# Kernel optimization log

Measured on AMD Instinct MI355X. Metric: run time of the kernel, lower is better.

Reference implementation:

```python
import jax, jax.numpy as jnp
import numpy as np

D_MODEL = 1024
N_HEADS = 16
N_KV_HEADS = 4
HEAD_DIM = 64   # d_model // total_n_heads
KEY_DIM = 64    # defaults to head_dim
N_REP = N_HEADS // N_KV_HEADS
ATTN_SCALE = 1.0 / np.sqrt(HEAD_DIM)
B, S = 2, 2048


def apply_rope(x, cos, sin):
    # x: [B,S,H,Dh]; cos/sin: [S,Dh//2]; pairs are (x[2j], x[2j+1]) per llama-style apply_rotary_emb
    xr, xi = x[..., ::2], x[..., 1::2]
    c = cos[None, :, None, :]
    s = sin[None, :, None, :]
    out_r = xr * c - xi * s
    out_i = xr * s + xi * c
    return jnp.stack([out_r, out_i], axis=-1).reshape(x.shape)


def setup_inputs() -> dict:
    key = jax.random.key(0)
    ks = jax.random.split(key, 7)
    query = jax.random.normal(ks[0], (B, S, D_MODEL), jnp.float32)
    k_in = jax.random.normal(ks[1], (B, S, D_MODEL), jnp.float32)
    v_in = jax.random.normal(ks[2], (B, S, D_MODEL), jnp.float32)
    # real RoPE frequency tables (theta=10000)
    inv_freq = 1.0 / (10000.0 ** (np.arange(0, KEY_DIM, 2, dtype=np.float32) / KEY_DIM))
    ang = np.outer(np.arange(S, dtype=np.float32), inv_freq)  # [S, KEY_DIM//2]
    freqs_cos = jnp.asarray(np.cos(ang), jnp.float32)
    freqs_sin = jnp.asarray(np.sin(ang), jnp.float32)
    sc = D_MODEL ** -0.5
    wq = jax.random.normal(ks[3], (N_HEADS * KEY_DIM, D_MODEL), jnp.float32) * sc
    wk = jax.random.normal(ks[4], (N_KV_HEADS * KEY_DIM, D_MODEL), jnp.float32) * sc
    wv = jax.random.normal(ks[5], (N_KV_HEADS * HEAD_DIM, D_MODEL), jnp.float32) * sc
    wo = jax.random.normal(ks[6], (N_HEADS * HEAD_DIM, N_HEADS * HEAD_DIM), jnp.float32) * sc
    return {"query": query, "key": k_in, "value": v_in,
            "freqs_cos": freqs_cos, "freqs_sin": freqs_sin,
            "wq": wq, "wk": wk, "wv": wv, "wo": wo}


def reference(query, key, value, freqs_cos, freqs_sin, wq, wk, wv, wo):
    b, sq, _ = query.shape
    sk = key.shape[1]
    xq = (query @ wq.T).reshape(b, sq, N_HEADS, KEY_DIM)
    xk = (key @ wk.T).reshape(b, sk, N_KV_HEADS, KEY_DIM)
    xv = (value @ wv.T).reshape(b, sk, N_KV_HEADS, HEAD_DIM)
    xq = apply_rope(xq, freqs_cos, freqs_sin)
    xk = apply_rope(xk, freqs_cos, freqs_sin)
    # GQA: repeat kv heads (equivalent to torch repeat_kv expand+reshape)
    xk = jnp.repeat(xk, N_REP, axis=2)
    xv = jnp.repeat(xv, N_REP, axis=2)
    scores = jnp.einsum('bqhd,bkhd->bhqk', xq, xk) * ATTN_SCALE
    causal = jnp.tril(jnp.ones((sq, sk), dtype=bool))
    scores = jnp.where(causal[None, None, :, :], scores, -jnp.inf)
    attn = jax.nn.softmax(scores, axis=-1)
    out = jnp.einsum('bhqk,bkhd->bqhd', attn, xv).reshape(b, sq, N_HEADS * HEAD_DIM)
    return out @ wo.T
```

## Files before the change

kernel.cpp:

```cpp
#include <hip/hip_runtime.h>

#define DM 1024
#define NHEADS 16
#define NKVH 4
#define HDIM 64
#define NB 2
#define SEQ 2048
#define MTOK (NB*SEQ)

typedef __attribute__((ext_vector_type(4))) float f32x4;
typedef __attribute__((ext_vector_type(8))) short short8;
typedef unsigned short u16;
typedef unsigned int u32;

__device__ __forceinline__ u16 f2b(float f) {
  u32 i; __builtin_memcpy(&i, &f, 4);
  u32 r = i + 0x7fffu + ((i >> 16) & 1u);
  return (u16)(r >> 16);
}
__device__ __forceinline__ u32 cvtpk(float a, float b) {
  u32 r; asm("v_cvt_pk_bf16_f32 %0, %1, %2" : "=v"(r) : "v"(a), "v"(b)); return r;
}
__device__ __forceinline__ float fexp2(float x) {
  float r; asm("v_exp_f32 %0, %1" : "=v"(r) : "v"(x)); return r;
}
__device__ __forceinline__ void gload16(const void* g, void* l) {
  __builtin_amdgcn_global_load_lds((const __attribute__((address_space(1))) u32*)g,
                                   (__attribute__((address_space(3))) u32*)l, 16, 0, 0);
}

__device__ __forceinline__ void cvt8(const float* __restrict__ src, u16* __restrict__ dst, int i) {
  float4 a = *(const float4*)(src + i);
  float4 b = *(const float4*)(src + i + 4);
  uint4 pk;
  pk.x = cvtpk(a.x, a.y);
  pk.y = cvtpk(a.z, a.w);
  pk.z = cvtpk(b.x, b.y);
  pk.w = cvtpk(b.z, b.w);
  *(uint4*)(dst + i) = pk;
}

__global__ __launch_bounds__(256) void cvt_all(const float* __restrict__ q, const float* __restrict__ k,
                                               const float* __restrict__ v, const float* __restrict__ wq,
                                               const float* __restrict__ wk, const float* __restrict__ wv,
                                               const float* __restrict__ wo, u16* oq, u16* ok, u16* ov,
                                               u16* owq, u16* owk, u16* owv, u16* owo) {
  const int ACT = (MTOK * DM) / 2048;
  const int BIG = (DM * DM) / 2048;
  const int SML = (256 * DM) / 2048;
  int bid = blockIdx.x;
  const float* s; u16* d;
  if (bid < ACT) { s = q; d = oq; }
  else if (bid < 2 * ACT) { s = k; d = ok; bid -= ACT; }
  else if (bid < 3 * ACT) { s = v; d = ov; bid -= 2 * ACT; }
  else {
    bid -= 3 * ACT;
    if (bid < BIG) { s = wq; d = owq; }
    else if (bid < 2 * BIG) { s = wo; d = owo; bid -= BIG; }
    else if (bid < 2 * BIG + SML) { s = wk; d = owk; bid -= 2 * BIG; }
    else { s = wv; d = owv; bid -= 2 * BIG + SML; }
  }
  cvt8(s, d, (bid * 256 + threadIdx.x) * 8);
}

template<int NR>
__device__ __forceinline__ void stage_tile(const u16* __restrict__ src, int k0, u16* lds,
                                           int w, int lane) {
#pragma unroll
  for (int i = 0; i < NR / 32; i++) {
    const int base = (i * 4 + w) * 1024;
    const int row = (base >> 7) + (lane >> 3);
    const int g = lane & 7;
    gload16(src + (size_t)row * DM + k0 + ((g ^ (row & 7)) << 3), (char*)lds + base);
  }
}
__device__ __forceinline__ short8 lds_frag(const u16* L, int row, int gr) {
  return *(const short8*)(L + row * 64 + ((gr ^ (row & 7)) << 3));
}

__global__ __launch_bounds__(256, 3) void gemm_qkv(const u16* __restrict__ Aq, const u16* __restrict__ Ak,
                                                   const u16* __restrict__ Av, const u16* __restrict__ wq,
                                                   const u16* __restrict__ wk, const u16* __restrict__ wv,
                                                   const float* __restrict__ cosb, const float* __restrict__ sinb,
                                                   u16* __restrict__ Qr, u16* __restrict__ Kr,
                                                   u16* __restrict__ Vt) {
  __shared__ __attribute__((aligned(16))) u16 SH[12288];
  u16* As = SH;
  u16* Bs = SH + 4096;
  const int tid = threadIdx.x, lane = tid & 63, w = tid >> 6;
  const int wr = w >> 1, wc = w & 1, lo = lane & 15, hi = lane >> 4;
  const int bx = blockIdx.x, by = blockIdx.y;
  const int m0 = bx * 64;

  const u16 *Ap, *Wp;
  int n0, mode;
  if (by < 8) { Ap = Aq; Wp = wq; n0 = by * 128; mode = 0; }
  else if (by < 10) { Ap = Ak; Wp = wk; n0 = (by - 8) * 128; mode = 1; }
  else { Ap = Av; Wp = wv; n0 = (by - 10) * 128; mode = 2; }
  const u16* Abase = Ap + (size_t)m0 * DM;
  const u16* Wbase = Wp + (size_t)n0 * DM;

  f32x4 acc[2][4];
#pragma unroll
  for (int i = 0; i < 2; i++)
#pragma unroll
    for (int j = 0; j < 4; j++) acc[i][j] = (f32x4){0.f, 0.f, 0.f, 0.f};

  for (int ks = 0; ks < 16; ks++) {
    const int k0 = ks * 64;
    stage_tile<64>(Abase, k0, As, w, lane);
    stage_tile<128>(Wbase, k0, Bs, w, lane);
    __syncthreads();
    short8 af[2][2], bfr[4][2];
#pragma unroll
    for (int mi = 0; mi < 2; mi++)
#pragma unroll
      for (int kk = 0; kk < 2; kk++)
        af[mi][kk] = lds_frag(As, wr * 32 + mi * 16 + lo, kk * 4 + hi);
#pragma unroll
    for (int ni = 0; ni < 4; ni++)
#pragma unroll
      for (int kk = 0; kk < 2; kk++)
        bfr[ni][kk] = lds_frag(Bs, wc * 64 + ni * 16 + lo, kk * 4 + hi);
    __builtin_amdgcn_s_setprio(1);
#pragma unroll
    for (int mi = 0; mi < 2; mi++)
#pragma unroll
      for (int ni = 0; ni < 4; ni++) {
        acc[mi][ni] = __builtin_amdgcn_mfma_f32_16x16x32_bf16(af[mi][0], bfr[ni][0], acc[mi][ni], 0, 0, 0);
        acc[mi][ni] = __builtin_amdgcn_mfma_f32_16x16x32_bf16(af[mi][1], bfr[ni][1], acc[mi][ni], 0, 0, 0);
      }
    __builtin_amdgcn_s_setprio(0);
    __syncthreads();
  }

  if (mode < 2) {
    const float scale = (mode == 0) ? 0.18033688f : 1.0f;
    u16* outp = (mode == 0) ? Qr : Kr;
    const int OH = (mode == 0) ? NHEADS : NKVH;
    const float sgn = (lo & 1) ? 1.0f : -1.0f;
#pragma unroll
    for (int ni = 0; ni < 4; ni++) {
      const int col = n0 + wc * 64 + ni * 16 + lo;
      const int h = col >> 6, d = col & 63, j = d >> 1;
#pragma unroll
      for (int mi = 0; mi < 2; mi++)
#pragma unroll
        for (int r = 0; r < 4; r++) {
          int row = m0 + wr * 32 + mi * 16 + hi * 4 + r;
          int srow = row & (SEQ - 1), bb = row >> 11;
          float v = acc[mi][ni][r];
          float pv = __shfl_xor(v, 1, 64);
          float c = cosb[srow * 32 + j];
          float s = sinb[srow * 32 + j];
          outp[((size_t)(bb * OH + h) * SEQ + srow) * 64 + d] = f2b((v * c + pv * s * sgn) * scale);
        }
    }
  } else {
    u16* Tt = SH;
#pragma unroll
    for (int mi = 0; mi < 2; mi++)
#pragma unroll
      for (int ni = 0; ni < 4; ni++) {
        const int cl = wc * 64 + ni * 16 + lo;
#pragma unroll
        for (int r = 0; r < 4; r++) {
          int rl = wr * 32 + mi * 16 + hi * 4 + r;
          Tt[cl * 72 + rl] = f2b(acc[mi][ni][r]);
        }
      }
    __syncthreads();
    const int dl = tid >> 1;
    const int sh2 = (tid & 1) * 32;
    const int dg = n0 + dl;
    const int kh = dg >> 6, drow = dg & 63;
    const int bb = m0 >> 11, sbase = m0 & (SEQ - 1);
    u16* dst = Vt + ((size_t)(bb * NKVH + kh) * 64 + drow) * SEQ + sbase + sh2;
#pragma unroll
    for (int i = 0; i < 4; i++)
      *(uint4*)(dst + i * 8) = *(const uint4*)&Tt[dl * 72 + sh2 + i * 8];
  }
}

__global__ __launch_bounds__(256, 4) void attn_kernel(const u16* __restrict__ Q, const u16* __restrict__ Kb,
                                                      const u16* __restrict__ Vt, u16* __restrict__ AO) {
  __shared__ __attribute__((aligned(16))) u16 SH[16384];
  const int tid = threadIdx.x;
  const int w = tid >> 6, lane = tid & 63;
  const int lo = lane & 15, hi = lane >> 4;
  const int bh = blockIdx.x;
  const int b = bh >> 4, h = bh & 15, kh = h >> 2;
  const int t = 31 - blockIdx.y;
  const int q0 = t * 64 + w * 16;
  const u16* Qp = Q + (size_t)bh * SEQ * 64;
  const u16* Kp = Kb + (size_t)(b * NKVH + kh) * SEQ * 64;
  const u16* Vp = Vt + (size_t)(b * NKVH + kh) * 64 * SEQ;

  short8 qf[2];
#pragma unroll
  for (int kk = 0; kk < 2; kk++)
    qf[kk] = *(const short8*)(Qp + (size_t)(q0 + lo) * 64 + kk * 32 + hi * 8);

  f32x4 o[4];
#pragma unroll
  for (int nf = 0; nf < 4; nf++) o[nf] = (f32x4){0.f, 0.f, 0.f, 0.f};
  float m = -__builtin_inff(), lsp = 0.f;

  auto key = [](int row) { return (row & 3) | (((row >> 3) & 1) << 2); };

  const u16* Ksrc0; const u16* Ksrc1; const u16* Vsrc0; const u16* Vsrc1;
  const int dst0 = w * 1024, dst1 = 4096 + w * 1024;
  {
    int byte0 = dst0 + (lane << 4);
    int row0 = byte0 >> 7;
    int gg0 = ((byte0 >> 4) & 7) ^ key(row0);
    Ksrc0 = Kp + row0 * 64 + gg0 * 8;
    Vsrc0 = Vp + (size_t)row0 * SEQ + gg0 * 8;
    int byte1 = dst1 + (lane << 4);
    int row1 = byte1 >> 7;
    int gg1 = ((byte1 >> 4) & 7) ^ key(row1);
    Ksrc1 = Kp + row1 * 64 + gg1 * 8;
    Vsrc1 = Vp + (size_t)row1 * SEQ + gg1 * 8;
  }
  auto stage2 = [&](int kv0, int bb) {
    gload16(Ksrc0 + kv0 * 64, (char*)SH + bb + dst0);
    gload16(Vsrc0 + kv0, (char*)SH + 16384 + bb + dst0);
    gload16(Ksrc1 + kv0 * 64, (char*)SH + bb + dst1);
    gload16(Vsrc1 + kv0, (char*)SH + 16384 + bb + dst1);
  };

  const int b3 = lo & 3;
  const int gx = hi ^ b3;
  const int kOffA = (8 * (lo >> 2) + b3) * 128 + gx * 16 + ((lo >> 2) & 1) * 64;
  const int kOffB = kOffA ^ 64;
  const int vOffA = lo * 128 + gx * 16 + ((lo >> 3) & 1) * 64;
  const int vOffB = vOffA ^ 64;
  const char* SHb = (const char*)SH;
  auto ld16 = [&](int off) { return *(const short8*)(SHb + off); };

  auto body = [&](int c, int kb , int nbb , bool pref, bool maskc) {
    if (pref) stage2((c + 1) * 64, nbb);
    short8 kf0[4], kf1[4];
    kf0[0] = ld16(kOffA + kb);        kf1[0] = ld16(kOffB + kb);
    kf0[1] = ld16(kOffA + kb + 512);  kf1[1] = ld16(kOffB + kb + 512);
    kf0[2] = ld16(kOffA + kb + 4096); kf1[2] = ld16(kOffB + kb + 4096);
    kf0[3] = ld16(kOffA + kb + 4608); kf1[3] = ld16(kOffB + kb + 4608);
    f32x4 sc[4];
#pragma unroll
    for (int f = 0; f < 4; f++) sc[f] = (f32x4){0.f, 0.f, 0.f, 0.f};
    __builtin_amdgcn_s_setprio(1);
#pragma unroll
    for (int f = 0; f < 4; f++) {
      sc[f] = __builtin_amdgcn_mfma_f32_16x16x32_bf16(kf0[f], qf[0], sc[f], 0, 0, 0);
      sc[f] = __builtin_amdgcn_mfma_f32_16x16x32_bf16(kf1[f], qf[1], sc[f], 0, 0, 0);
    }
    __builtin_amdgcn_s_setprio(0);
    short8 vb0[4], vb1[4];
#pragma unroll
    for (int nf = 0; nf < 4; nf++) {
      vb0[nf] = ld16(vOffA + kb + 16384 + nf * 2048);
      vb1[nf] = ld16(vOffB + kb + 16384 + nf * 2048);
    }
    if (maskc) {
      const int kv0 = c * 64;
#pragma unroll
      for (int f = 0; f < 4; f++) {
        int kvb = kv0 + 32 * (f >> 1) + 8 * hi + 4 * (f & 1);
#pragma unroll
        for (int r = 0; r < 4; r++)
          if (kvb + r > q0 + lo) sc[f][r] = -__builtin_inff();
      }
    }
    float t0 = fmaxf(fmaxf(sc[0][0], sc[0][1]), fmaxf(sc[0][2], sc[0][3]));
    float t1 = fmaxf(fmaxf(sc[1][0], sc[1][1]), fmaxf(sc[1][2], sc[1][3]));
    float t2 = fmaxf(fmaxf(sc[2][0], sc[2][1]), fmaxf(sc[2][2], sc[2][3]));
    float t3 = fmaxf(fmaxf(sc[3][0], sc[3][1]), fmaxf(sc[3][2], sc[3][3]));
    float lm = fmaxf(fmaxf(t0, t1), fmaxf(t2, t3));
    if (__any(lm - m > 8.f)) {
      float mx = fmaxf(m, lm);
      mx = fmaxf(mx, __shfl_xor(mx, 16, 64));
      mx = fmaxf(mx, __shfl_xor(mx, 32, 64));
      float corr = fexp2(m - mx);
      m = mx;
      lsp *= corr;
      float corrq[4];
#pragma unroll
      for (int r = 0; r < 4; r++) corrq[r] = __shfl(corr, hi * 4 + r, 64);
#pragma unroll
      for (int nf = 0; nf < 4; nf++)
#pragma unroll
        for (int r = 0; r < 4; r++) o[nf][r] *= corrq[r];
    }
    float pv2[4][4];
    float ps[4];
#pragma unroll
    for (int f = 0; f < 4; f++) {
#pragma unroll
      for (int r = 0; r < 4; r++) pv2[f][r] = fexp2(sc[f][r] - m);
      ps[f] = (pv2[f][0] + pv2[f][1]) + (pv2[f][2] + pv2[f][3]);
    }
    lsp += (ps[0] + ps[1]) + (ps[2] + ps[3]);
    union { u32 u[4]; short8 s8; } pa0, pa1;
#pragma unroll
    for (int tt = 0; tt < 4; tt++) {
      int fsel = tt >> 1, r0 = 2 * (tt & 1);
      pa0.u[tt] = cvtpk(pv2[fsel][r0], pv2[fsel][r0 + 1]);
      pa1.u[tt] = cvtpk(pv2[2 + fsel][r0], pv2[2 + fsel][r0 + 1]);
    }
    __builtin_amdgcn_s_setprio(1);
#pragma unroll
    for (int nf = 0; nf < 4; nf++) {
      o[nf] = __builtin_amdgcn_mfma_f32_16x16x32_bf16(pa0.s8, vb0[nf], o[nf], 0, 0, 0);
      o[nf] = __builtin_amdgcn_mfma_f32_16x16x32_bf16(pa1.s8, vb1[nf], o[nf], 0, 0, 0);
    }
    __builtin_amdgcn_s_setprio(0);
    __syncthreads();
  };

  stage2(0, 0);
  __syncthreads();

  int c = 0;
  for (; c + 2 <= t; c += 2) {
    body(c, 0, 8192, true, false);
    body(c + 1, 8192, 0, true, false);
  }
  if (c < t) {
    body(c, 0, 8192, true, false);
    body(c + 1, 8192, 0, false, true);
  } else {
    body(c, 0, 8192, false, true);
  }

  lsp += __shfl_xor(lsp, 16, 64);
  lsp += __shfl_xor(lsp, 32, 64);
  float inv = 1.0f / lsp;
  float invq[4];
#pragma unroll
  for (int r = 0; r < 4; r++) invq[r] = __shfl(inv, hi * 4 + r, 64);
#pragma unroll
  for (int nf = 0; nf < 4; nf++)
#pragma unroll
    for (int r = 0; r < 4; r++) {
      int q = q0 + hi * 4 + r;
      int d = nf * 16 + lo;
      AO[((size_t)(b * SEQ + q) * NHEADS + h) * 64 + d] = f2b(o[nf][r] * invq[r]);
    }
}

__global__ __launch_bounds__(256, 2) void gemm_out(const u16* __restrict__ A, const u16* __restrict__ W,
                                                   float* __restrict__ Out) {
  __shared__ __attribute__((aligned(16))) u16 SH[12288];
  u16* As = SH;
  u16* Bs = SH + 4096;
  const int tid = threadIdx.x, lane = tid & 63, w = tid >> 6;
  const int wr = w >> 1, wc = w & 1, lo = lane & 15, hi = lane >> 4;
  const int m0 = blockIdx.x * 64, n0 = blockIdx.y * 128;
  const u16* Abase = A + (size_t)m0 * DM;
  const u16* Wbase = W + (size_t)n0 * DM;

  f32x4 acc[2][4];
#pragma unroll
  for (int i = 0; i < 2; i++)
#pragma unroll
    for (int j = 0; j < 4; j++) acc[i][j] = (f32x4){0.f, 0.f, 0.f, 0.f};

  for (int ks = 0; ks < 16; ks++) {
    const int k0 = ks * 64;
    stage_tile<64>(Abase, k0, As, w, lane);
    stage_tile<128>(Wbase, k0, Bs, w, lane);
    __syncthreads();
    short8 af[2][2], bfr[4][2];
#pragma unroll
    for (int mi = 0; mi < 2; mi++)
#pragma unroll
      for (int kk = 0; kk < 2; kk++)
        af[mi][kk] = lds_frag(As, wr * 32 + mi * 16 + lo, kk * 4 + hi);
#pragma unroll
    for (int ni = 0; ni < 4; ni++)
#pragma unroll
      for (int kk = 0; kk < 2; kk++)
        bfr[ni][kk] = lds_frag(Bs, wc * 64 + ni * 16 + lo, kk * 4 + hi);
    __builtin_amdgcn_s_setprio(1);
#pragma unroll
    for (int mi = 0; mi < 2; mi++)
#pragma unroll
      for (int ni = 0; ni < 4; ni++) {
        acc[mi][ni] = __builtin_amdgcn_mfma_f32_16x16x32_bf16(af[mi][0], bfr[ni][0], acc[mi][ni], 0, 0, 0);
        acc[mi][ni] = __builtin_amdgcn_mfma_f32_16x16x32_bf16(af[mi][1], bfr[ni][1], acc[mi][ni], 0, 0, 0);
      }
    __builtin_amdgcn_s_setprio(0);
    __syncthreads();
  }

#pragma unroll
  for (int mi = 0; mi < 2; mi++)
#pragma unroll
    for (int ni = 0; ni < 4; ni++)
#pragma unroll
      for (int r = 0; r < 4; r++) {
        int row = m0 + wr * 32 + mi * 16 + hi * 4 + r;
        int col = n0 + wc * 64 + ni * 16 + lo;
        Out[(size_t)row * DM + col] = acc[mi][ni][r];
      }
}

extern "C" void kernel_launch(void* const* d_in, const int* in_sizes, int n_in,
                              void* d_out, int out_size, void* d_ws, size_t ws_size,
                              hipStream_t stream) {
  const float* query = (const float*)d_in[0];
  const float* key_ = (const float*)d_in[1];
  const float* value = (const float*)d_in[2];
  const float* fcos = (const float*)d_in[3];
  const float* fsin = (const float*)d_in[4];
  const float* wq = (const float*)d_in[5];
  const float* wk = (const float*)d_in[6];
  const float* wv = (const float*)d_in[7];
  const float* wo = (const float*)d_in[8];

  char* ws = (char*)d_ws;
  size_t off = 0;
  auto alloc = [&](size_t elems) {
    u16* p = (u16*)(ws + off);
    off = (off + elems * 2 + 255) & ~(size_t)255;
    return p;
  };
  u16* qf = alloc((size_t)MTOK * DM);
  u16* kf = alloc((size_t)MTOK * DM);
  u16* vf = alloc((size_t)MTOK * DM);
  u16* wqf = alloc((size_t)DM * DM);
  u16* wkf = alloc((size_t)256 * DM);
  u16* wvf = alloc((size_t)256 * DM);
  u16* wof = alloc((size_t)DM * DM);
  u16* Qr = alloc((size_t)MTOK * DM);
  u16* Kr = alloc((size_t)NB * NKVH * SEQ * 64);
  u16* Vt = alloc((size_t)NB * NKVH * 64 * SEQ);
  u16* AO = alloc((size_t)MTOK * DM);

  cvt_all<<<3 * 2048 + 1280, 256, 0, stream>>>(query, key_, value, wq, wk, wv, wo,
                                               qf, kf, vf, wqf, wkf, wvf, wof);

  gemm_qkv<<<dim3(64, 12), 256, 0, stream>>>(qf, kf, vf, wqf, wkf, wvf,
                                             fcos, fsin, Qr, Kr, Vt);

  attn_kernel<<<dim3(NB * NHEADS, 32), 256, 0, stream>>>(Qr, Kr, Vt, AO);

  gemm_out<<<dim3(64, 8), 256, 0, stream>>>(AO, wof, (float*)d_out);
}
```

Baseline: 83.75 us.

## Pair mirrored causal query tiles per block to balance work and share K/V loads

Each attention block now processes two query tiles, p and 31-p, reusing every staged K/V chunk for both. This equalizes causal work across blocks and halves K/V shared-memory staging per query tile. The grid shrinks to 16 in y and launch bounds drop to 2 blocks per CU because register pressure roughly doubles. The masking value changes from -inf to a large negative finite value.

```diff
diff --git a/kernel.cpp b/kernel.cpp
--- a/kernel.cpp
+++ b/kernel.cpp
@@ -7,6 +7,7 @@
 #define NB 2
 #define SEQ 2048
 #define MTOK (NB*SEQ)
+#define NEGS (-1e30f)
 
 typedef __attribute__((ext_vector_type(4))) float f32x4;
 typedef __attribute__((ext_vector_type(8))) short short8;
@@ -182,7 +183,54 @@
   }
 }
 
-__global__ __launch_bounds__(256, 4) void attn_kernel(const u16* __restrict__ Q, const u16* __restrict__ Kb,
+__device__ __forceinline__ void softpv(f32x4 (&sc)[4], float& m, float& lsp, f32x4 (&o)[4],
+                                       const short8 (&vb0)[4], const short8 (&vb1)[4], int hi) {
+  float t0 = fmaxf(fmaxf(sc[0][0], sc[0][1]), fmaxf(sc[0][2], sc[0][3]));
+  float t1 = fmaxf(fmaxf(sc[1][0], sc[1][1]), fmaxf(sc[1][2], sc[1][3]));
+  float t2 = fmaxf(fmaxf(sc[2][0], sc[2][1]), fmaxf(sc[2][2], sc[2][3]));
+  float t3 = fmaxf(fmaxf(sc[3][0], sc[3][1]), fmaxf(sc[3][2], sc[3][3]));
+  float lm = fmaxf(fmaxf(t0, t1), fmaxf(t2, t3));
+  if (__any(lm - m > 8.f)) {
+    float mx = fmaxf(m, lm);
+    mx = fmaxf(mx, __shfl_xor(mx, 16, 64));
+    mx = fmaxf(mx, __shfl_xor(mx, 32, 64));
+    float corr = fexp2(m - mx);
+    m = mx;
+    lsp *= corr;
+    float corrq[4];
+#pragma unroll
+    for (int r = 0; r < 4; r++) corrq[r] = __shfl(corr, hi * 4 + r, 64);
+#pragma unroll
+    for (int nf = 0; nf < 4; nf++)
+#pragma unroll
+      for (int r = 0; r < 4; r++) o[nf][r] *= corrq[r];
+  }
+  float pv2[4][4];
+  float ps[4];
+#pragma unroll
+  for (int f = 0; f < 4; f++) {
+#pragma unroll
+    for (int r = 0; r < 4; r++) pv2[f][r] = fexp2(sc[f][r] - m);
+    ps[f] = (pv2[f][0] + pv2[f][1]) + (pv2[f][2] + pv2[f][3]);
+  }
+  lsp += (ps[0] + ps[1]) + (ps[2] + ps[3]);
+  union { u32 u[4]; short8 s8; } pa0, pa1;
+#pragma unroll
+  for (int tt = 0; tt < 4; tt++) {
+    int fsel = tt >> 1, r0 = 2 * (tt & 1);
+    pa0.u[tt] = cvtpk(pv2[fsel][r0], pv2[fsel][r0 + 1]);
+    pa1.u[tt] = cvtpk(pv2[2 + fsel][r0], pv2[2 + fsel][r0 + 1]);
+  }
+  __builtin_amdgcn_s_setprio(1);
+#pragma unroll
+  for (int nf = 0; nf < 4; nf++) {
+    o[nf] = __builtin_amdgcn_mfma_f32_16x16x32_bf16(pa0.s8, vb0[nf], o[nf], 0, 0, 0);
+    o[nf] = __builtin_amdgcn_mfma_f32_16x16x32_bf16(pa1.s8, vb1[nf], o[nf], 0, 0, 0);
+  }
+  __builtin_amdgcn_s_setprio(0);
+}
+
+__global__ __launch_bounds__(256, 2) void attn_kernel(const u16* __restrict__ Q, const u16* __restrict__ Kb,
                                                       const u16* __restrict__ Vt, u16* __restrict__ AO) {
   __shared__ __attribute__((aligned(16))) u16 SH[16384];
   const int tid = threadIdx.x;
@@ -190,21 +238,26 @@
   const int lo = lane & 15, hi = lane >> 4;
   const int bh = blockIdx.x;
   const int b = bh >> 4, h = bh & 15, kh = h >> 2;
-  const int t = 31 - blockIdx.y;
-  const int q0 = t * 64 + w * 16;
+  const int p = blockIdx.y;
+  const int tA = p, tB = 31 - p;
+  const int q0A = tA * 64 + w * 16;
+  const int q0B = tB * 64 + w * 16;
   const u16* Qp = Q + (size_t)bh * SEQ * 64;
   const u16* Kp = Kb + (size_t)(b * NKVH + kh) * SEQ * 64;
   const u16* Vp = Vt + (size_t)(b * NKVH + kh) * 64 * SEQ;
 
-  short8 qf[2];
-#pragma unroll
-  for (int kk = 0; kk < 2; kk++)
-    qf[kk] = *(const short8*)(Qp + (size_t)(q0 + lo) * 64 + kk * 32 + hi * 8);
-
-  f32x4 o[4];
-#pragma unroll
-  for (int nf = 0; nf < 4; nf++) o[nf] = (f32x4){0.f, 0.f, 0.f, 0.f};
-  float m = -__builtin_inff(), lsp = 0.f;
+  short8 qfA[2], qfB[2];
+#pragma unroll
+  for (int kk = 0; kk < 2; kk++) {
+    qfA[kk] = *(const short8*)(Qp + (size_t)(q0A + lo) * 64 + kk * 32 + hi * 8);
+    qfB[kk] = *(const short8*)(Qp + (size_t)(q0B + lo) * 64 + kk * 32 + hi * 8);
+  }
+
+  f32x4 oA[4], oB[4];
+#pragma unroll
+  for (int nf = 0; nf < 4; nf++) { oA[nf] = (f32x4){0.f,0.f,0.f,0.f}; oB[nf] = (f32x4){0.f,0.f,0.f,0.f}; }
+  float mA = NEGS, lspA = 0.f;
+  float mB = NEGS, lspB = 0.f;
 
   auto key = [](int row) { return (row & 3) | (((row >> 3) & 1) << 2); };
 
@@ -238,114 +291,105 @@
   const char* SHb = (const char*)SH;
   auto ld16 = [&](int off) { return *(const short8*)(SHb + off); };
 
-  auto body = [&](int c, int kb , int nbb , bool pref, bool maskc) {
-    if (pref) stage2((c + 1) * 64, nbb);
-    short8 kf0[4], kf1[4];
-    kf0[0] = ld16(kOffA + kb);        kf1[0] = ld16(kOffB + kb);
-    kf0[1] = ld16(kOffA + kb + 512);  kf1[1] = ld16(kOffB + kb + 512);
-    kf0[2] = ld16(kOffA + kb + 4096); kf1[2] = ld16(kOffB + kb + 4096);
-    kf0[3] = ld16(kOffA + kb + 4608); kf1[3] = ld16(kOffB + kb + 4608);
-    f32x4 sc[4];
-#pragma unroll
-    for (int f = 0; f < 4; f++) sc[f] = (f32x4){0.f, 0.f, 0.f, 0.f};
-    __builtin_amdgcn_s_setprio(1);
-#pragma unroll
-    for (int f = 0; f < 4; f++) {
-      sc[f] = __builtin_amdgcn_mfma_f32_16x16x32_bf16(kf0[f], qf[0], sc[f], 0, 0, 0);
-      sc[f] = __builtin_amdgcn_mfma_f32_16x16x32_bf16(kf1[f], qf[1], sc[f], 0, 0, 0);
-    }
-    __builtin_amdgcn_s_setprio(0);
-    short8 vb0[4], vb1[4];
-#pragma unroll
-    for (int nf = 0; nf < 4; nf++) {
-      vb0[nf] = ld16(vOffA + kb + 16384 + nf * 2048);
-      vb1[nf] = ld16(vOffB + kb + 16384 + nf * 2048);
-    }
-    if (maskc) {
-      const int kv0 = c * 64;
-#pragma unroll
-      for (int f = 0; f < 4; f++) {
-        int kvb = kv0 + 32 * (f >> 1) + 8 * hi + 4 * (f & 1);
-#pragma unroll
-        for (int r = 0; r < 4; r++)
-          if (kvb + r > q0 + lo) sc[f][r] = -__builtin_inff();
-      }
-    }
-    float t0 = fmaxf(fmaxf(sc[0][0], sc[0][1]), fmaxf(sc[0][2], sc[0][3]));
-    float t1 = fmaxf(fmaxf(sc[1][0], sc[1][1]), fmaxf(sc[1][2], sc[1][3]));
-    float t2 = fmaxf(fmaxf(sc[2][0], sc[2][1]), fmaxf(sc[2][2], sc[2][3]));
-    float t3 = fmaxf(fmaxf(sc[3][0], sc[3][1]), fmaxf(sc[3][2], sc[3][3]));
-    float lm = fmaxf(fmaxf(t0, t1), fmaxf(t2, t3));
-    if (__any(lm - m > 8.f)) {
-      float mx = fmaxf(m, lm);
-      mx = fmaxf(mx, __shfl_xor(mx, 16, 64));
-      mx = fmaxf(mx, __shfl_xor(mx, 32, 64));
-      float corr = fexp2(m - mx);
-      m = mx;
-      lsp *= corr;
-      float corrq[4];
-#pragma unroll
-      for (int r = 0; r < 4; r++) corrq[r] = __shfl(corr, hi * 4 + r, 64);
-#pragma unroll
-      for (int nf = 0; nf < 4; nf++)
-#pragma unroll
-        for (int r = 0; r < 4; r++) o[nf][r] *= corrq[r];
-    }
-    float pv2[4][4];
-    float ps[4];
-#pragma unroll
-    for (int f = 0; f < 4; f++) {
-#pragma unroll
-      for (int r = 0; r < 4; r++) pv2[f][r] = fexp2(sc[f][r] - m);
-      ps[f] = (pv2[f][0] + pv2[f][1]) + (pv2[f][2] + pv2[f][3]);
-    }
-    lsp += (ps[0] + ps[1]) + (ps[2] + ps[3]);
-    union { u32 u[4]; short8 s8; } pa0, pa1;
-#pragma unroll
-    for (int tt = 0; tt < 4; tt++) {
-      int fsel = tt >> 1, r0 = 2 * (tt & 1);
-      pa0.u[tt] = cvtpk(pv2[fsel][r0], pv2[fsel][r0 + 1]);
-      pa1.u[tt] = cvtpk(pv2[2 + fsel][r0], pv2[2 + fsel][r0 + 1]);
-    }
-    __builtin_amdgcn_s_setprio(1);
-#pragma unroll
-    for (int nf = 0; nf < 4; nf++) {
-      o[nf] = __builtin_amdgcn_mfma_f32_16x16x32_bf16(pa0.s8, vb0[nf], o[nf], 0, 0, 0);
-      o[nf] = __builtin_amdgcn_mfma_f32_16x16x32_bf16(pa1.s8, vb1[nf], o[nf], 0, 0, 0);
-    }
-    __builtin_amdgcn_s_setprio(0);
-    __syncthreads();
-  };
+#define CHUNK(CC, KB, NBB, PREF, LAST)                                                      \
+  do {                                                                                      \
+    const int c_ = (CC);                                                                    \
+    if (PREF) stage2((c_ + 1) * 64, (NBB));                                                 \
+    short8 kf0[4], kf1[4];                                                                  \
+    kf0[0] = ld16(kOffA + (KB));        kf1[0] = ld16(kOffB + (KB));                        \
+    kf0[1] = ld16(kOffA + (KB) + 512);  kf1[1] = ld16(kOffB + (KB) + 512);                  \
+    kf0[2] = ld16(kOffA + (KB) + 4096); kf1[2] = ld16(kOffB + (KB) + 4096);                 \
+    kf0[3] = ld16(kOffA + (KB) + 4608); kf1[3] = ld16(kOffB + (KB) + 4608);                 \
+    const bool actA = (c_ <= tA);                                                           \
+    f32x4 scA[4], scB[4];                                                                   \
+    _Pragma("unroll")                                                                       \
+    for (int f = 0; f < 4; f++) scB[f] = (f32x4){0.f, 0.f, 0.f, 0.f};                       \
+    __builtin_amdgcn_s_setprio(1);                                                          \
+    _Pragma("unroll")                                                                       \
+    for (int f = 0; f < 4; f++) {                                                           \
+      scB[f] = __builtin_amdgcn_mfma_f32_16x16x32_bf16(kf0[f], qfB[0], scB[f], 0, 0, 0);    \
+      scB[f] = __builtin_amdgcn_mfma_f32_16x16x32_bf16(kf1[f], qfB[1], scB[f], 0, 0, 0);    \
+    }                                                                                       \
+    __builtin_amdgcn_s_setprio(0);                                                          \
+    if (actA) {                                                                             \
+      _Pragma("unroll")                                                                     \
+      for (int f = 0; f < 4; f++) scA[f] = (f32x4){0.f, 0.f, 0.f, 0.f};                     \
+      __builtin_amdgcn_s_setprio(1);                                                        \
+      _Pragma("unroll")                                                                     \
+      for (int f = 0; f < 4; f++) {                                                         \
+        scA[f] = __builtin_amdgcn_mfma_f32_16x16x32_bf16(kf0[f], qfA[0], scA[f], 0, 0, 0);  \
+        scA[f] = __builtin_amdgcn_mfma_f32_16x16x32_bf16(kf1[f], qfA[1], scA[f], 0, 0, 0);  \
+      }                                                                                     \
+      __builtin_amdgcn_s_setprio(0);                                                        \
+    }                                                                                       \
+    short8 vb0[4], vb1[4];                                                                  \
+    _Pragma("unroll")                                                                       \
+    for (int nf = 0; nf < 4; nf++) {                                                        \
+      vb0[nf] = ld16(vOffA + (KB) + 16384 + nf * 2048);                                     \
+      vb1[nf] = ld16(vOffB + (KB) + 16384 + nf * 2048);                                     \
+    }                                                                                       \
+    const int kv0_ = c_ * 64;                                                               \
+    if (LAST) {                                                                             \
+      _Pragma("unroll")                                                                     \
+      for (int f = 0; f < 4; f++) {                                                         \
+        int kvb = kv0_ + 32 * (f >> 1) + 8 * hi + 4 * (f & 1);                              \
+        _Pragma("unroll")                                                                   \
+        for (int r = 0; r < 4; r++)                                                         \
+          if (kvb + r > q0B + lo) scB[f][r] = NEGS;                                         \
+      }                                                                                     \
+    }                                                                                       \
+    softpv(scB, mB, lspB, oB, vb0, vb1, hi);                                                \
+    if (actA) {                                                                             \
+      if (c_ == tA) {                                                                       \
+        _Pragma("unroll")                                                                   \
+        for (int f = 0; f < 4; f++) {                                                       \
+          int kvb = kv0_ + 32 * (f >> 1) + 8 * hi + 4 * (f & 1);                            \
+          _Pragma("unroll")                                                                 \
+          for (int r = 0; r < 4; r++)                                                       \
+            if (kvb + r > q0A + lo) scA[f][r] = NEGS;                                       \
+        }                                                                                   \
+      }                                                                                     \
+      softpv(scA, mA, lspA, oA, vb0, vb1, hi);                                              \
+    }                                                                                       \
+    __syncthreads();                                                                        \
+  } while (0)
 
   stage2(0, 0);
   __syncthreads();
 
   int c = 0;
-  for (; c + 2 <= t; c += 2) {
-    body(c, 0, 8192, true, false);
-    body(c + 1, 8192, 0, true, false);
-  }
-  if (c < t) {
-    body(c, 0, 8192, true, false);
-    body(c + 1, 8192, 0, false, true);
+  for (; c + 2 <= tB; c += 2) {
+    CHUNK(c, 0, 8192, true, false);
+    CHUNK(c + 1, 8192, 0, true, false);
+  }
+  if (c < tB) {
+    CHUNK(c, 0, 8192, true, false);
+    CHUNK(c + 1, 8192, 0, false, true);
   } else {
-    body(c, 0, 8192, false, true);
-  }
-
-  lsp += __shfl_xor(lsp, 16, 64);
-  lsp += __shfl_xor(lsp, 32, 64);
-  float inv = 1.0f / lsp;
-  float invq[4];
-#pragma unroll
-  for (int r = 0; r < 4; r++) invq[r] = __shfl(inv, hi * 4 + r, 64);
-#pragma unroll
-  for (int nf = 0; nf < 4; nf++)
-#pragma unroll
-    for (int r = 0; r < 4; r++) {
-      int q = q0 + hi * 4 + r;
-      int d = nf * 16 + lo;
-      AO[((size_t)(b * SEQ + q) * NHEADS + h) * 64 + d] = f2b(o[nf][r] * invq[r]);
-    }
+    CHUNK(c, 0, 8192, false, true);
+  }
+#undef CHUNK
+
+#pragma unroll
+  for (int t2 = 0; t2 < 2; t2++) {
+    float lsp = t2 ? lspB : lspA;
+    const int q0 = t2 ? q0B : q0A;
+    f32x4* o = t2 ? oB : oA;
+    lsp += __shfl_xor(lsp, 16, 64);
+    lsp += __shfl_xor(lsp, 32, 64);
+    float inv = 1.0f / lsp;
+    float invq[4];
+#pragma unroll
+    for (int r = 0; r < 4; r++) invq[r] = __shfl(inv, hi * 4 + r, 64);
+#pragma unroll
+    for (int nf = 0; nf < 4; nf++)
+#pragma unroll
+      for (int r = 0; r < 4; r++) {
+        int q = q0 + hi * 4 + r;
+        int d = nf * 16 + lo;
+        AO[((size_t)(b * SEQ + q) * NHEADS + h) * 64 + d] = f2b(o[nf][r] * invq[r]);
+      }
+  }
 }
 
 __global__ __launch_bounds__(256, 2) void gemm_out(const u16* __restrict__ A, const u16* __restrict__ W,
@@ -443,7 +487,7 @@
   gemm_qkv<<<dim3(64, 12), 256, 0, stream>>>(qf, kf, vf, wqf, wkf, wvf,
                                              fcos, fsin, Qr, Kr, Vt);
 
-  attn_kernel<<<dim3(NB * NHEADS, 32), 256, 0, stream>>>(Qr, Kr, Vt, AO);
+  attn_kernel<<<dim3(NB * NHEADS, 16), 256, 0, stream>>>(Qr, Kr, Vt, AO);
 
   gemm_out<<<dim3(64, 8), 256, 0, stream>>>(AO, wof, (float*)d_out);
 }
```

New measurement: 83.44 us (median of 2 runs). About the same (-0.4%).
